# Kernel tuning notes

Hardware: AMD Instinct MI355X
Metric: run time of the kernel (lower is better)

The kernel has to match this reference:

```python
import jax, jax.numpy as jnp
import numpy as np

COMMITMENT_COST = 0.25
NUM_EMBEDDINGS = 4096
EMBEDDING_DIM = 256


def setup_inputs() -> dict:
    key = jax.random.key(0)
    kx, ke = jax.random.split(key)
    x = jax.random.normal(kx, (64, 1024, EMBEDDING_DIM), dtype=jnp.float32)
    # nn.Embedding weight initialized uniform(-1/K, 1/K)
    emb = jax.random.uniform(ke, (NUM_EMBEDDINGS, EMBEDDING_DIM), dtype=jnp.float32,
                             minval=-1.0 / NUM_EMBEDDINGS, maxval=1.0 / NUM_EMBEDDINGS)
    return {"x": x, "emb": emb}


def reference(x, emb):
    D = emb.shape[1]
    flat_x = x.reshape(-1, D)                                    # [N, D]
    distances = (jnp.sum(flat_x * flat_x, axis=1, keepdims=True)
                 - 2.0 * flat_x @ emb.T
                 + jnp.sum(emb * emb, axis=1))
    indices = jnp.argmin(distances, axis=1)                      # [N]
    quantized = emb[indices].reshape(x.shape)                    # [..., D]
    e_latent_loss = jnp.mean((jax.lax.stop_gradient(quantized) - x) ** 2)
    q_latent_loss = jnp.mean((quantized - jax.lax.stop_gradient(x)) ** 2)
    loss = q_latent_loss + COMMITMENT_COST * e_latent_loss
    # straight-through estimator
    quantized = x + jax.lax.stop_gradient(quantized - x)
    return quantized, loss, indices[:, None]
```

## Files before the change

kernel.cpp:

```cpp
#include <hip/hip_runtime.h>
#include <math.h>

#define DIMD 256
#define KCODES 4096
#define NROWS 65536
#define QN (NROWS * DIMD)

constexpr int P1_BM = 64;
constexpr int P1_BN = 128;
constexpr int NT    = KCODES / P1_BN;
constexpr int NCHUNK = NT * 2;
constexpr float TAU2 = 7.5e-4f;
constexpr float TAU2B = TAU2 + 1e-5f;
constexpr int CAP   = 48;

typedef __attribute__((ext_vector_type(8))) short bf16x8;
typedef __attribute__((ext_vector_type(4))) float f32x4;

#define VM8() asm volatile("s_waitcnt vmcnt(8)" ::: "memory")
#define VM0() asm volatile("s_waitcnt vmcnt(0)" ::: "memory")

__device__ __forceinline__ unsigned short f2bf(float f) {
    unsigned int u = __builtin_bit_cast(unsigned int, f);
    u += 0x7fffu + ((u >> 16) & 1u);
    return (unsigned short)(u >> 16);
}

__device__ __forceinline__ float opaque(float v) {
    asm volatile("" : "+v"(v));
    return v;
}

__device__ __forceinline__ void gload_lds16(const void* g, void* l) {
    __builtin_amdgcn_global_load_lds(
        (const __attribute__((address_space(1))) unsigned int*)g,
        (__attribute__((address_space(3))) unsigned int*)l, 16, 0, 0);
}

__device__ __forceinline__ float keyf(unsigned int w) {
    return __builtin_bit_cast(float, w & 0xFFFFF000u);
}

__global__ void sx_kernel(const float* __restrict__ x, float* __restrict__ sx) {
    const int j   = threadIdx.x & 7;
    const int row = blockIdx.x * 32 + (threadIdx.x >> 3);
    const float* p = x + (size_t)row * DIMD;
    float total = 0.0f;
    #pragma unroll
    for (int half = 0; half < 2; ++half) {
        const float* b = p + half * 128;
        const float v0 = b[j];
        float r = opaque(v0 * v0);
        #pragma unroll
        for (int i = 8; i < 128; i += 8) {
            const float v = b[i + j];
            r += opaque(v * v);
        }
        const float s1  = r  + __shfl_xor(r, 1, 64);
        const float s2  = s1 + __shfl_xor(s1, 2, 64);
        const float res = s2 + __shfl_xor(s2, 4, 64);
        total = (half == 0) ? res : (total + res);
    }
    if (j == 0) sx[row] = total;
}

__global__ void se_kernel(const float* __restrict__ emb, float* __restrict__ se) {
    const int j   = threadIdx.x & 7;
    const int row = blockIdx.x * 32 + (threadIdx.x >> 3);
    const float* p = emb + (size_t)row * DIMD;
    float total = 0.0f;
    #pragma unroll
    for (int half = 0; half < 2; ++half) {
        const float* b = p + half * 128;
        const float v0 = b[j];
        float r = opaque(v0 * v0);
        #pragma unroll
        for (int i = 8; i < 128; i += 8) {
            const float v = b[i + j];
            r += opaque(v * v);
        }
        const float s1  = r  + __shfl_xor(r, 1, 64);
        const float s2  = s1 + __shfl_xor(s1, 2, 64);
        const float res = s2 + __shfl_xor(s2, 4, 64);
        total = (half == 0) ? res : (total + res);
    }
    if (j == 0) se[row] = total;
}

__global__ void conv_emb_kernel(const float* __restrict__ emb, unsigned short* __restrict__ embh) {
    const int i = blockIdx.x * blockDim.x + threadIdx.x;
    const float4 v = ((const float4*)emb)[i];
    ushort4 h;
    h.x = f2bf(v.x); h.y = f2bf(v.y); h.z = f2bf(v.z); h.w = f2bf(v.w);
    ((ushort4*)embh)[i] = h;
}

__global__ __launch_bounds__(256, 2)
void pass1_kernel(const float* __restrict__ x, const unsigned short* __restrict__ embh,
                  unsigned int* __restrict__ cand, int* __restrict__ cnt_out) {
    __shared__ unsigned short Bs[2][16384];
    __shared__ unsigned int cand_lds[P1_BM * CAP];
    __shared__ float part[4][32];
    __shared__ float tilemax[P1_BM];
    __shared__ int   cnts[P1_BM];

    const int t    = threadIdx.x;
    const int w    = t >> 6;
    const int lane = t & 63;
    const int quad = lane >> 4;
    const int lm   = lane & 15;
    const int wr   = w >> 1;
    const int wc   = w & 1;
    const int row0 = blockIdx.x * P1_BM;

    if (t < P1_BM) cnts[t] = 0;

    bf16x8 afr[2][8];
    #pragma unroll
    for (int f = 0; f < 2; ++f) {
        const float* xr = x + (size_t)(row0 + wr * 32 + f * 16 + lm) * DIMD + quad * 8;
        #pragma unroll
        for (int c = 0; c < 8; ++c) {
            const float4 v0 = *(const float4*)(xr + c * 32);
            const float4 v1 = *(const float4*)(xr + c * 32 + 4);
            bf16x8 h;
            h[0] = (short)f2bf(v0.x); h[1] = (short)f2bf(v0.y);
            h[2] = (short)f2bf(v0.z); h[3] = (short)f2bf(v0.w);
            h[4] = (short)f2bf(v1.x); h[5] = (short)f2bf(v1.y);
            h[6] = (short)f2bf(v1.z); h[7] = (short)f2bf(v1.w);
            afr[f][c] = h;
        }
    }

    auto stage = [&](int buf, int m) {
        const int c0  = (m >> 1) * P1_BN;
        const int kcb = (m & 1) * 128;
        #pragma unroll
        for (int i = 0; i < 8; ++i) {
            const int seg = i * 4 + w;
            const int c   = seg * 4 + (lane >> 4);
            const int kk  = ((lane & 15) ^ (c & 15)) * 8;
            const unsigned short* src = embh + (size_t)(c0 + c) * DIMD + kcb + kk;
            gload_lds16(src, &Bs[buf][seg * 512]);
        }
    };

    stage(0, 0);
    int buf = 0;

    float rmg[2][4];
    #pragma unroll
    for (int f = 0; f < 2; ++f)
        #pragma unroll
        for (int reg = 0; reg < 4; ++reg) rmg[f][reg] = -INFINITY;

    for (int tile = 0; tile < NT; ++tile) {
        const int c0 = tile * P1_BN;
        f32x4 acc[2][4];
        #pragma unroll
        for (int f = 0; f < 2; ++f)
            #pragma unroll
            for (int g = 0; g < 4; ++g) acc[f][g] = (f32x4){0.f, 0.f, 0.f, 0.f};

        #pragma unroll
        for (int kb = 0; kb < 2; ++kb) {
            const int m = tile * 2 + kb;
            __syncthreads();
            if (m + 1 < NCHUNK) {
                stage(buf ^ 1, m + 1);
                VM8();
            } else {
                VM0();
            }
            __syncthreads();

            #pragma unroll
            for (int ks = 0; ks < 4; ++ks) {
                bf16x8 b[4];
                #pragma unroll
                for (int g = 0; g < 4; ++g) {
                    const int c = wc * 64 + g * 16 + lm;
                    b[g] = *(const bf16x8*)
                        &Bs[buf][c * 128 + ((((ks << 2) + quad) ^ lm) << 3)];
                }
                #pragma unroll
                for (int f = 0; f < 2; ++f)
                    #pragma unroll
                    for (int g = 0; g < 4; ++g)
                        acc[f][g] = __builtin_amdgcn_mfma_f32_16x16x32_bf16(
                            afr[f][kb * 4 + ks], b[g], acc[f][g], 0, 0, 0);
            }
            buf ^= 1;
        }

        #pragma unroll
        for (int f = 0; f < 2; ++f) {
            f32x4 mm4;
            #pragma unroll
            for (int reg = 0; reg < 4; ++reg) {
                float mm = fmaxf(fmaxf(acc[f][0][reg], acc[f][1][reg]),
                                 fmaxf(acc[f][2][reg], acc[f][3][reg]));
                #pragma unroll
                for (int off = 1; off < 16; off <<= 1)
                    mm = fmaxf(mm, __shfl_xor(mm, off, 64));
                mm4[reg] = mm;
            }
            if (lm == 0)
                *(f32x4*)&part[w][f * 16 + quad * 4] = mm4;
        }

        __syncthreads();
        if (t < P1_BM) {
            const int trg = t >> 5, loc = t & 31;
            tilemax[t] = fmaxf(part[trg * 2][loc], part[trg * 2 + 1][loc]);
        }
        __syncthreads();

        #pragma unroll
        for (int f = 0; f < 2; ++f) {
            const f32x4 tm = *(const f32x4*)&tilemax[wr * 32 + f * 16 + quad * 4];
            #pragma unroll
            for (int reg = 0; reg < 4; ++reg) {
                rmg[f][reg] = fmaxf(rmg[f][reg], tm[reg]);
                const float thr = rmg[f][reg] - TAU2;
                const int r = wr * 32 + f * 16 + quad * 4 + reg;
                #pragma unroll
                for (int g = 0; g < 4; ++g) {
                    const float dv = acc[f][g][reg];
                    if (dv > thr) {
                        const int slot = atomicAdd(&cnts[r], 1);
                        if (slot < CAP) {
                            const unsigned int ub =
                                __builtin_bit_cast(unsigned int, fmaxf(dv, 0.0f));
                            cand_lds[r * CAP + slot] =
                                (ub & 0xFFFFF000u) |
                                (unsigned int)(c0 + wc * 64 + g * 16 + lm);
                        }
                    }
                }
            }
        }
    }
    __syncthreads();

    {
        const int r = t & 63;
        #pragma unroll
        for (int s = t >> 6; s < CAP; s += 4)
            cand[(size_t)s * NROWS + row0 + r] = cand_lds[r * CAP + s];
    }
    if (t < P1_BM) cnt_out[row0 + t] = (cnts[t] > CAP) ? -1 : cnts[t];
}

__global__ __launch_bounds__(256, 4)
void pass2_kernel(const float* __restrict__ x, const float* __restrict__ emb,
                  const float* __restrict__ sx, const float* __restrict__ se,
                  const unsigned int* __restrict__ cand, const int* __restrict__ cnt,
                  float* __restrict__ out, float* __restrict__ partial) {
    __shared__ int idx_lds[64];
    __shared__ int wl[64];
    __shared__ int ovf[64];
    __shared__ int counts[2];
    const int t = threadIdx.x;
    const int w = t >> 6, lane = t & 63;
    const int row0 = blockIdx.x * 64;

    if (t < 2) counts[t] = 0;
    __syncthreads();

    if (t < 64) {
        const int row = row0 + t;
        const int n = cnt[row];
        if (n < 0) {
            ovf[atomicAdd(&counts[1], 1)] = t;
        } else {
            unsigned int kw[16];
            #pragma unroll
            for (int s = 0; s < 16; ++s)
                kw[s] = cand[(size_t)s * NROWS + row];
            float mx = -INFINITY;
            #pragma unroll
            for (int s = 0; s < 16; ++s)
                if (s < n) mx = fmaxf(mx, keyf(kw[s]));
            for (int s = 16; s < n; ++s)
                mx = fmaxf(mx, keyf(cand[(size_t)s * NROWS + row]));
            const float thr = mx - TAU2B;
            int nsurv = 0, scode = 0;
            #pragma unroll
            for (int s = 0; s < 16; ++s)
                if (s < n && keyf(kw[s]) > thr) { ++nsurv; scode = (int)(kw[s] & 0xFFFu); }
            for (int s = 16; s < n; ++s) {
                const unsigned int wd = cand[(size_t)s * NROWS + row];
                if (keyf(wd) > thr) { ++nsurv; scode = (int)(wd & 0xFFFu); }
            }
            if (nsurv == 1) idx_lds[t] = scode;
            else            wl[atomicAdd(&counts[0], 1)] = t;
        }
    }
    __syncthreads();
    const int nwl = counts[0], novf = counts[1];

    if (t < nwl) {
        const int lr = wl[t];
        const int row = row0 + lr;
        const int n = cnt[row];
        const float sxr = sx[row];
        float mx = -INFINITY;
        for (int s = 0; s < n; ++s)
            mx = fmaxf(mx, keyf(cand[(size_t)s * NROWS + row]));
        const float thr = mx - TAU2B;
        float bestd = INFINITY; int bestc = 0x7fffffff;
        const float4* xp4 = (const float4*)(x + (size_t)row * DIMD);
        for (int s = 0; s < n; ++s) {
            const unsigned int wd = cand[(size_t)s * NROWS + row];
            if (keyf(wd) > thr) {
                const int code = (int)(wd & 0xFFFu);
                const float4* ep4 = (const float4*)(emb + (size_t)code * DIMD);
                float a = 0.0f;
                #pragma unroll
                for (int d4 = 0; d4 < DIMD / 4; ++d4) {
                    const float4 xv = xp4[d4];
                    const float4 ev = ep4[d4];
                    a = fmaf(xv.x, ev.x, a);
                    a = fmaf(xv.y, ev.y, a);
                    a = fmaf(xv.z, ev.z, a);
                    a = fmaf(xv.w, ev.w, a);
                }
                const float t1 = sxr - 2.0f * a;
                const float dd = t1 + se[code];
                if (dd < bestd || (dd == bestd && code < bestc)) { bestd = dd; bestc = code; }
            }
        }
        idx_lds[lr] = bestc;
    }

    for (int i = w; i < novf; i += 4) {
        const int lr = ovf[i];
        const int row = row0 + lr;
        const float sxr = sx[row];
        const float4* xp4 = (const float4*)(x + (size_t)row * DIMD);
        float bestd = INFINITY; int bestc = 0x7fffffff;
        for (int c = lane; c < KCODES; c += 64) {
            const float4* ep4 = (const float4*)(emb + (size_t)c * DIMD);
            float a = 0.0f;
            for (int d4 = 0; d4 < DIMD / 4; ++d4) {
                const float4 xv = xp4[d4];
                const float4 ev = ep4[d4];
                a = fmaf(xv.x, ev.x, a);
                a = fmaf(xv.y, ev.y, a);
                a = fmaf(xv.z, ev.z, a);
                a = fmaf(xv.w, ev.w, a);
            }
            const float t1 = sxr - 2.0f * a;
            const float dd = t1 + se[c];
            if (dd < bestd || (dd == bestd && c < bestc)) { bestd = dd; bestc = c; }
        }
        #pragma unroll
        for (int off = 32; off > 0; off >>= 1) {
            const float od = __shfl_down(bestd, off, 64);
            const int   oc = __shfl_down(bestc, off, 64);
            if (od < bestd || (od == bestd && oc < bestc)) { bestd = od; bestc = oc; }
        }
        if (lane == 0) idx_lds[lr] = bestc;
    }
    __syncthreads();

    for (int r = w; r < 64; r += 4) {
        const int row = row0 + r;
        const int code = idx_lds[r];
        const float4 xv = ((const float4*)(x + (size_t)row * DIMD))[lane];
        const float4 ev = ((const float4*)(emb + (size_t)code * DIMD))[lane];
        ((float4*)(out + (size_t)row * DIMD))[lane] = ev;
        const float dx = ev.x - xv.x, dy = ev.y - xv.y,
                    dz = ev.z - xv.z, dw = ev.w - xv.w;
        float s = dx * dx + dy * dy + dz * dz + dw * dw;
        #pragma unroll
        for (int off = 32; off > 0; off >>= 1) s += __shfl_down(s, off, 64);
        if (lane == 0) {
            partial[row] = s;
            out[QN + 1 + row] = (float)code;
        }
    }
}

__global__ void loss_reduce_kernel(const float* __restrict__ partial, float* __restrict__ out) {
    const int t = threadIdx.x;
    double s = 0.0;
    for (int i = t; i < NROWS; i += 256) s += (double)partial[i];
    __shared__ double tsum[256];
    tsum[t] = s;
    __syncthreads();
    #pragma unroll
    for (int off = 128; off > 0; off >>= 1) {
        if (t < off) tsum[t] += tsum[t + off];
        __syncthreads();
    }
    if (t == 0) out[QN] = (float)(tsum[0] * (1.25 / (double)QN));
}

extern "C" void kernel_launch(void* const* d_in, const int* in_sizes, int n_in,
                              void* d_out, int out_size, void* d_ws, size_t ws_size,
                              hipStream_t stream) {
    const float* x   = (const float*)d_in[0];
    const float* emb = (const float*)d_in[1];
    float* out = (float*)d_out;

    char* ws = (char*)d_ws;
    unsigned short* embh = (unsigned short*)ws;           ws += (size_t)KCODES * DIMD * 2;
    float* sx  = (float*)ws;                              ws += (size_t)NROWS * 4;
    float* se  = (float*)ws;                              ws += (size_t)KCODES * 4;
    unsigned int* cand = (unsigned int*)ws;               ws += (size_t)NROWS * CAP * 4;
    int*   cnt  = (int*)ws;                               ws += (size_t)NROWS * 4;
    float* partial = (float*)ws;

    conv_emb_kernel<<<KCODES * DIMD / 4 / 256, 256, 0, stream>>>(emb, embh);
    sx_kernel<<<NROWS / 32, 256, 0, stream>>>(x, sx);
    se_kernel<<<KCODES / 32, 256, 0, stream>>>(emb, se);
    pass1_kernel<<<NROWS / P1_BM, 256, 0, stream>>>(x, embh, cand, cnt);
    pass2_kernel<<<NROWS / 64, 256, 0, stream>>>(x, emb, sx, se, cand, cnt, out, partial);
    loss_reduce_kernel<<<1, 256, 0, stream>>>(partial, out);
}
```

Baseline: 898.3 us.

## Fuse candidate rescoring into pass1, keeping candidates and x rows in LDS

Merges the pass2 rescoring and output stage into the pass1 kernel. Candidate lists stay in shared memory with a padded stride, and the per-row running max is reused, so the global candidate buffer round trip and second launch go away. The block's x rows are staged into the freed B-tile LDS with an XOR swizzle for the exact fp32 rescoring and output. In exchange, the rescoring tail now runs at pass1's lower occupancy of 2 blocks per CU instead of 4, and LDS use grows slightly.

```diff
diff --git a/kernel.cpp b/kernel.cpp
--- a/kernel.cpp
+++ b/kernel.cpp
@@ -12,7 +12,8 @@
 constexpr int NCHUNK = NT * 2;
 constexpr float TAU2 = 7.5e-4f;
 constexpr float TAU2B = TAU2 + 1e-5f;
-constexpr int CAP   = 48;
+constexpr int CAP  = 48;
+constexpr int CAPS = 49;
 
 typedef __attribute__((ext_vector_type(8))) short bf16x8;
 typedef __attribute__((ext_vector_type(4))) float f32x4;
@@ -97,12 +98,19 @@
 
 __global__ __launch_bounds__(256, 2)
 void pass1_kernel(const float* __restrict__ x, const unsigned short* __restrict__ embh,
-                  unsigned int* __restrict__ cand, int* __restrict__ cnt_out) {
-    __shared__ unsigned short Bs[2][16384];
-    __shared__ unsigned int cand_lds[P1_BM * CAP];
+                  const float* __restrict__ emb, const float* __restrict__ sx,
+                  const float* __restrict__ se, float* __restrict__ out,
+                  float* __restrict__ partial) {
+    __shared__ __align__(16) unsigned short Bs[2][16384];
+    __shared__ unsigned int cand_lds[P1_BM * CAPS];
     __shared__ float part[4][32];
     __shared__ float tilemax[P1_BM];
+    __shared__ float finalmax[P1_BM];
     __shared__ int   cnts[P1_BM];
+    __shared__ int   idx_lds[P1_BM];
+    __shared__ int   wl[P1_BM];
+    __shared__ int   ovf[P1_BM];
+    __shared__ int   cnt2[2];
 
     const int t    = threadIdx.x;
     const int w    = t >> 6;
@@ -114,6 +122,7 @@
     const int row0 = blockIdx.x * P1_BM;
 
     if (t < P1_BM) cnts[t] = 0;
+    if (t < 2) cnt2[t] = 0;
 
     bf16x8 afr[2][8];
     #pragma unroll
@@ -232,7 +241,7 @@
                         if (slot < CAP) {
                             const unsigned int ub =
                                 __builtin_bit_cast(unsigned int, fmaxf(dv, 0.0f));
-                            cand_lds[r * CAP + slot] =
+                            cand_lds[r * CAPS + slot] =
                                 (ub & 0xFFFFF000u) |
                                 (unsigned int)(c0 + wc * 64 + g * 16 + lm);
                         }
@@ -243,83 +252,54 @@
     }
     __syncthreads();
 
-    {
-        const int r = t & 63;
-        #pragma unroll
-        for (int s = t >> 6; s < CAP; s += 4)
-            cand[(size_t)s * NROWS + row0 + r] = cand_lds[r * CAP + s];
-    }
-    if (t < P1_BM) cnt_out[row0 + t] = (cnts[t] > CAP) ? -1 : cnts[t];
-}
-
-__global__ __launch_bounds__(256, 4)
-void pass2_kernel(const float* __restrict__ x, const float* __restrict__ emb,
-                  const float* __restrict__ sx, const float* __restrict__ se,
-                  const unsigned int* __restrict__ cand, const int* __restrict__ cnt,
-                  float* __restrict__ out, float* __restrict__ partial) {
-    __shared__ int idx_lds[64];
-    __shared__ int wl[64];
-    __shared__ int ovf[64];
-    __shared__ int counts[2];
-    const int t = threadIdx.x;
-    const int w = t >> 6, lane = t & 63;
-    const int row0 = blockIdx.x * 64;
-
-    if (t < 2) counts[t] = 0;
-    __syncthreads();
-
-    if (t < 64) {
-        const int row = row0 + t;
-        const int n = cnt[row];
-        if (n < 0) {
-            ovf[atomicAdd(&counts[1], 1)] = t;
+    if (wc == 0 && lm == 0) {
+        #pragma unroll
+        for (int f = 0; f < 2; ++f)
+            #pragma unroll
+            for (int reg = 0; reg < 4; ++reg)
+                finalmax[wr * 32 + f * 16 + quad * 4 + reg] = rmg[f][reg];
+    }
+    float4* xs4 = (float4*)&Bs[0][0];
+    for (int rr = w * 16; rr < w * 16 + 16; ++rr) {
+        const float4 xv = ((const float4*)(x + (size_t)(row0 + rr) * DIMD))[lane];
+        xs4[rr * 64 + (lane ^ rr)] = xv;
+    }
+    __syncthreads();
+
+    if (t < P1_BM) {
+        const int n = cnts[t];
+        if (n > CAP) {
+            ovf[atomicAdd(&cnt2[1], 1)] = t;
         } else {
-            unsigned int kw[16];
-            #pragma unroll
-            for (int s = 0; s < 16; ++s)
-                kw[s] = cand[(size_t)s * NROWS + row];
-            float mx = -INFINITY;
-            #pragma unroll
-            for (int s = 0; s < 16; ++s)
-                if (s < n) mx = fmaxf(mx, keyf(kw[s]));
-            for (int s = 16; s < n; ++s)
-                mx = fmaxf(mx, keyf(cand[(size_t)s * NROWS + row]));
-            const float thr = mx - TAU2B;
+            const float thr = finalmax[t] - TAU2B;
             int nsurv = 0, scode = 0;
-            #pragma unroll
-            for (int s = 0; s < 16; ++s)
-                if (s < n && keyf(kw[s]) > thr) { ++nsurv; scode = (int)(kw[s] & 0xFFFu); }
-            for (int s = 16; s < n; ++s) {
-                const unsigned int wd = cand[(size_t)s * NROWS + row];
+            for (int s = 0; s < n; ++s) {
+                const unsigned int wd = cand_lds[t * CAPS + s];
                 if (keyf(wd) > thr) { ++nsurv; scode = (int)(wd & 0xFFFu); }
             }
             if (nsurv == 1) idx_lds[t] = scode;
-            else            wl[atomicAdd(&counts[0], 1)] = t;
-        }
-    }
-    __syncthreads();
-    const int nwl = counts[0], novf = counts[1];
+            else            wl[atomicAdd(&cnt2[0], 1)] = t;
+        }
+    }
+    __syncthreads();
+    const int nwl = cnt2[0], novf = cnt2[1];
 
     if (t < nwl) {
         const int lr = wl[t];
         const int row = row0 + lr;
-        const int n = cnt[row];
+        const int n = cnts[lr];
         const float sxr = sx[row];
-        float mx = -INFINITY;
-        for (int s = 0; s < n; ++s)
-            mx = fmaxf(mx, keyf(cand[(size_t)s * NROWS + row]));
-        const float thr = mx - TAU2B;
+        const float thr = finalmax[lr] - TAU2B;
         float bestd = INFINITY; int bestc = 0x7fffffff;
-        const float4* xp4 = (const float4*)(x + (size_t)row * DIMD);
         for (int s = 0; s < n; ++s) {
-            const unsigned int wd = cand[(size_t)s * NROWS + row];
+            const unsigned int wd = cand_lds[lr * CAPS + s];
             if (keyf(wd) > thr) {
                 const int code = (int)(wd & 0xFFFu);
                 const float4* ep4 = (const float4*)(emb + (size_t)code * DIMD);
                 float a = 0.0f;
                 #pragma unroll
                 for (int d4 = 0; d4 < DIMD / 4; ++d4) {
-                    const float4 xv = xp4[d4];
+                    const float4 xv = xs4[lr * 64 + (d4 ^ lr)];
                     const float4 ev = ep4[d4];
                     a = fmaf(xv.x, ev.x, a);
                     a = fmaf(xv.y, ev.y, a);
@@ -338,13 +318,12 @@
         const int lr = ovf[i];
         const int row = row0 + lr;
         const float sxr = sx[row];
-        const float4* xp4 = (const float4*)(x + (size_t)row * DIMD);
         float bestd = INFINITY; int bestc = 0x7fffffff;
         for (int c = lane; c < KCODES; c += 64) {
             const float4* ep4 = (const float4*)(emb + (size_t)c * DIMD);
             float a = 0.0f;
             for (int d4 = 0; d4 < DIMD / 4; ++d4) {
-                const float4 xv = xp4[d4];
+                const float4 xv = xs4[lr * 64 + (d4 ^ lr)];
                 const float4 ev = ep4[d4];
                 a = fmaf(xv.x, ev.x, a);
                 a = fmaf(xv.y, ev.y, a);
@@ -365,11 +344,11 @@
     }
     __syncthreads();
 
-    for (int r = w; r < 64; r += 4) {
+    for (int r = w; r < P1_BM; r += 4) {
         const int row = row0 + r;
         const int code = idx_lds[r];
-        const float4 xv = ((const float4*)(x + (size_t)row * DIMD))[lane];
         const float4 ev = ((const float4*)(emb + (size_t)code * DIMD))[lane];
+        const float4 xv = xs4[r * 64 + (lane ^ r)];
         ((float4*)(out + (size_t)row * DIMD))[lane] = ev;
         const float dx = ev.x - xv.x, dy = ev.y - xv.y,
                     dz = ev.z - xv.z, dw = ev.w - xv.w;
@@ -409,14 +388,11 @@
     unsigned short* embh = (unsigned short*)ws;           ws += (size_t)KCODES * DIMD * 2;
     float* sx  = (float*)ws;                              ws += (size_t)NROWS * 4;
     float* se  = (float*)ws;                              ws += (size_t)KCODES * 4;
-    unsigned int* cand = (unsigned int*)ws;               ws += (size_t)NROWS * CAP * 4;
-    int*   cnt  = (int*)ws;                               ws += (size_t)NROWS * 4;
     float* partial = (float*)ws;
 
     conv_emb_kernel<<<KCODES * DIMD / 4 / 256, 256, 0, stream>>>(emb, embh);
     sx_kernel<<<NROWS / 32, 256, 0, stream>>>(x, sx);
     se_kernel<<<KCODES / 32, 256, 0, stream>>>(emb, se);
-    pass1_kernel<<<NROWS / P1_BM, 256, 0, stream>>>(x, embh, cand, cnt);
-    pass2_kernel<<<NROWS / 64, 256, 0, stream>>>(x, emb, sx, se, cand, cnt, out, partial);
+    pass1_kernel<<<NROWS / P1_BM, 256, 0, stream>>>(x, embh, emb, sx, se, out, partial);
     loss_reduce_kernel<<<1, 256, 0, stream>>>(partial, out);
 }
```

Result: no change. 912.2 us (+1.6%).
